# Kernel tuning notes

Measured on AMD Instinct MI355X. Metric: run time of the kernel, lower is better.

The kernel has to match this reference:

```python
import jax, jax.numpy as jnp
import numpy as np

B, T, T3, P = 512, 128, 64, 12
IN1, H1 = 64, 256
IN2, H2 = 64, 256
IN3, H3 = 32, 128
GLOB, OUT = 32, 2
FC_IN = 2 * H1 + H2 + GLOB + 2 * P * H3  # 3872


def lstm_last(x, Wih, Whh, bih, bhh):
    """Single-layer batch-first LSTM (PyTorch gate order i,f,g,o); returns last hidden state [B,H]."""
    Bx = x.shape[0]
    H = Whh.shape[1]
    # precompute input projections for all timesteps: [T, B, 4H]
    xg = jnp.swapaxes(jnp.einsum('bti,gi->btg', x, Wih) + bih + bhh, 0, 1)

    def step(carry, g):
        h, c = carry
        gates = g + h @ Whh.T
        i, f, gg, o = jnp.split(gates, 4, axis=-1)
        c = jax.nn.sigmoid(f) * c + jax.nn.sigmoid(i) * jnp.tanh(gg)
        h = jax.nn.sigmoid(o) * jnp.tanh(c)
        return (h, c), None

    h0 = jnp.zeros((Bx, H), x.dtype)
    (h, _), _ = jax.lax.scan(step, (h0, h0), xg)
    return h


def setup_inputs() -> dict:
    key = jax.random.key(0)
    ks = jax.random.split(key, 20)
    n = lambda k, s: jax.random.normal(k, s, dtype=jnp.float32)
    w = lambda k, s: jax.random.normal(k, s, dtype=jnp.float32) * 0.05
    return {
        'current_game': n(ks[0], (B, GLOB)),
        'games_home': n(ks[1], (B, T, IN1)),
        'games_away': n(ks[2], (B, T, IN1)),
        'games_vs': n(ks[3], (B, T, IN2)),
        'players_home': n(ks[4], (B, P, T3, IN3)),
        'players_away': n(ks[5], (B, P, T3, IN3)),
        'Wih1': w(ks[6], (4 * H1, IN1)), 'Whh1': w(ks[7], (4 * H1, H1)),
        'bih1': w(ks[8], (4 * H1,)), 'bhh1': w(ks[9], (4 * H1,)),
        'Wih2': w(ks[10], (4 * H2, IN2)), 'Whh2': w(ks[11], (4 * H2, H2)),
        'bih2': w(ks[12], (4 * H2,)), 'bhh2': w(ks[13], (4 * H2,)),
        'Wih3': w(ks[14], (4 * H3, IN3)), 'Whh3': w(ks[15], (4 * H3, H3)),
        'bih3': w(ks[16], (4 * H3,)), 'bhh3': w(ks[17], (4 * H3,)),
        'Wfc': w(ks[18], (OUT, FC_IN)), 'bfc': w(ks[19], (OUT,)),
    }


def reference(current_game, games_home, games_away, games_vs, players_home, players_away,
              Wih1, Whh1, bih1, bhh1, Wih2, Whh2, bih2, bhh2, Wih3, Whh3, bih3, bhh3,
              Wfc, bfc):
    h_home = lstm_last(games_home, Wih1, Whh1, bih1, bhh1)   # [B, H1]
    h_away = lstm_last(games_away, Wih1, Whh1, bih1, bhh1)   # shared rnn weights
    h_vs = lstm_last(games_vs, Wih2, Whh2, bih2, bhh2)       # [B, H2]

    def players_feat(xp):
        # fold the player dim into batch: one batched LSTM pass instead of P launches
        b, p = xp.shape[0], xp.shape[1]
        h = lstm_last(xp.reshape(b * p, xp.shape[2], xp.shape[3]), Wih3, Whh3, bih3, bhh3)
        return h.reshape(b, p * H3)  # concat in player order, matching the torch loop

    feat = jnp.concatenate([
        h_home, h_away, h_vs,
        players_feat(players_home), players_feat(players_away),
        current_game,
    ], axis=1)  # [B, FC_IN]
    return feat @ Wfc.T + bfc
```

## Files before the change

### kernel.cpp

```cpp
#include <hip/hip_runtime.h>
#include <stdint.h>

typedef __bf16 bf16;
typedef bf16 bf16x8 __attribute__((ext_vector_type(8)));
typedef bf16 bf16x4 __attribute__((ext_vector_type(4)));
typedef float f32x4 __attribute__((ext_vector_type(4)));
typedef int i32x4 __attribute__((ext_vector_type(4)));

#define DEV __device__ __forceinline__

static const size_t OFF_W1 = 0;
static const size_t OFF_W2 = OFF_W1 + (size_t)640 * 1024;
static const size_t OFF_W3 = OFF_W2 + (size_t)640 * 1024;
static const size_t OFF_B1 = OFF_W3 + (size_t)160 * 1024;
static const size_t OFF_B2 = OFF_B1 + 4096;
static const size_t OFF_B3 = OFF_B2 + 4096;
static const size_t OFF_FEAT = OFF_B3 + 2048;
static const size_t WS_NEEDED = OFF_FEAT + (size_t)512 * 3840 * 4;

DEV float sigm(float x) { return 1.f / (1.f + __expf(-x)); }
DEV float tanh_(float x) { return 1.f - 2.f / (__expf(2.f * x) + 1.f); }

DEV void mfma_bv(f32x4& acc, i32x4 a, i32x4 b) {
  asm("v_mfma_f32_16x16x32_bf16 %0, %1, %2, %0" : "+a"(acc) : "v"(a), "v"(b));
}
DEV void mfma_ba(f32x4& acc, i32x4 a, i32x4 b) {
  asm("v_mfma_f32_16x16x32_bf16 %0, %1, %2, %0" : "+a"(acc) : "v"(a), "a"(b));
}

template <int H, int IN, int NT, int NKT>
DEV void packW(const float* __restrict__ Wih, const float* __restrict__ Whh,
               bf16* __restrict__ dst, int i) {
  int e = i & 7, lane = (i >> 3) & 63;
  int rest = i >> 9;
  int kt = rest % NKT; rest /= NKT;
  int nt = rest % NT;  int w = rest / NT;
  int quad = lane >> 4, l16 = lane & 15;
  constexpr int NTG = NT / 4, UW = NT * 4;
  int unit = w * UW + (nt % NTG) * 16 + l16;
  int g = nt / NTG;
  int r = g * H + unit;
  int k = kt * 32 + quad * 8 + e;
  float v = (k < IN) ? Wih[r * IN + k] : Whh[r * H + (k - IN)];
  dst[i] = (bf16)v;
}

__global__ void prep_kernel(const float* __restrict__ Wih1, const float* __restrict__ Whh1,
                            const float* __restrict__ bih1, const float* __restrict__ bhh1,
                            const float* __restrict__ Wih2, const float* __restrict__ Whh2,
                            const float* __restrict__ bih2, const float* __restrict__ bhh2,
                            const float* __restrict__ Wih3, const float* __restrict__ Whh3,
                            const float* __restrict__ bih3, const float* __restrict__ bhh3,
                            uint8_t* __restrict__ ws) {
  const int gt = blockIdx.x * blockDim.x + threadIdx.x;
  const int gs = gridDim.x * blockDim.x;
  bf16* W1 = (bf16*)(ws + OFF_W1);
  bf16* W2 = (bf16*)(ws + OFF_W2);
  bf16* W3 = (bf16*)(ws + OFF_W3);
  float* B1 = (float*)(ws + OFF_B1);
  float* B2 = (float*)(ws + OFF_B2);
  float* B3 = (float*)(ws + OFF_B3);
  for (int i = gt; i < 640 * 512; i += gs) {
    packW<256, 64, 16, 10>(Wih1, Whh1, W1, i);
    packW<256, 64, 16, 10>(Wih2, Whh2, W2, i);
  }
  for (int i = gt; i < 160 * 512; i += gs) packW<128, 32, 8, 5>(Wih3, Whh3, W3, i);
  for (int i = gt; i < 1024; i += gs) { B1[i] = bih1[i] + bhh1[i]; B2[i] = bih2[i] + bhh2[i]; }
  for (int i = gt; i < 512; i += gs) B3[i] = bih3[i] + bhh3[i];
}

template <int BM, int IN, int H, int T, int NT, int NKT, int NVV, int NVA, int NL, int NS,
          int DOM>
DEV void lstm_tile3(const float* __restrict__ x0, const float* __restrict__ x1, int halfM,
                    const bf16* __restrict__ Wd, const float* __restrict__ bsum,
                    float* __restrict__ feat, int mg, uint8_t* smem) {
  static_assert(NVV + NVA + NL + NS == NT, "split");
  static_assert((NL == 0 && NS == 0) || (NKT % 2 == 0), "wrap parity");
  constexpr int MT = BM / 16;
  constexpr int NTG = NT / 4;
  constexpr int UW = NT * 4;
  constexpr int KCH = (IN + H) / 8;
  constexpr int SROW = KCH + 1;
  constexpr int AROWE = SROW * 8;
  constexpr int XPT = BM * IN / 4 / 256;

  const int tid = threadIdx.x;
  const int lane = tid & 63;
  const int w = tid >> 6;
  const int quad = lane >> 4;
  const int l16 = lane & 15;
  const int rowbase = mg * BM;

  bf16* A = (bf16*)smem;
  bf16* Wshm = (bf16*)(smem + (size_t)BM * AROWE * 2);

  const float* xb = (rowbase < halfM) ? x0 : x1;
  const int rowoff = rowbase - ((rowbase < halfM) ? 0 : halfM);

  {
    constexpr int HCH = KCH - IN / 8;
    for (int i = tid; i < BM * HCH * 4; i += 256) {
      int row = i / (HCH * 4), rem = i % (HCH * 4);
      int chunk = IN / 8 + rem / 4, d = rem % 4;
      ((uint32_t*)A)[row * SROW * 4 + chunk * 4 + d] = 0;
    }
  }
  if constexpr (NL > 0) {
    for (int idx = tid; idx < 4 * NL * NKT * 64; idx += 256) {
      int ln = idx & 63;
      int kt = (idx >> 6) % NKT;
      int rest = (idx >> 6) / NKT;
      int nl = rest % NL, w2 = rest / NL;
      int blob = (w2 * NT + NVV + NVA + nl) * NKT + kt;
      *(bf16x8*)(Wshm + (size_t)((w2 * NL + nl) * NKT + kt) * 512 + ln * 8) =
          *(const bf16x8*)(Wd + (size_t)blob * 512 + ln * 8);
    }
  }
  i32x4 wregv[NVV > 0 ? NVV : 1][NKT];
  {
    const bf16* Wv = Wd + (size_t)(w * NT) * NKT * 512 + lane * 8;
#pragma unroll
    for (int nt = 0; nt < NVV; ++nt)
#pragma unroll
      for (int kt = 0; kt < NKT; ++kt)
        wregv[nt][kt] = *(const i32x4*)(Wv + (size_t)(nt * NKT + kt) * 512);
  }
  i32x4 wrega[NVA > 0 ? NVA : 1][NKT];
  {
    const bf16* Wa = Wd + (size_t)(w * NT + NVV) * NKT * 512 + lane * 8;
#pragma unroll
    for (int nt = 0; nt < NVA; ++nt)
#pragma unroll
      for (int kt = 0; kt < NKT; ++kt)
        wrega[nt][kt] = *(const i32x4*)(Wa + (size_t)(nt * NKT + kt) * 512);
  }
  const bf16* Wstream = Wd + (size_t)(w * NT + NVV + NVA + NL) * NKT * 512 + lane * 8;

  float bias[4][NTG];
#pragma unroll
  for (int g = 0; g < 4; ++g)
#pragma unroll
    for (int ut = 0; ut < NTG; ++ut)
      bias[g][ut] = bsum[g * H + w * UW + ut * 16 + l16];

  i32x4 sbuf[2][NS > 0 ? NS : 1];
  i32x4 wlds[2][NL > 0 ? NL : 1];

  float4 xr[XPT];
#pragma unroll
  for (int i = 0; i < XPT; ++i) {
    int idx = i * 256 + tid;
    int row = idx / (IN / 4), c4 = idx % (IN / 4);
    xr[i] = *(const float4*)(xb + (size_t)(rowoff + row) * T * IN + c4 * 4);
  }
#pragma unroll
  for (int i = 0; i < XPT; ++i) {
    int idx = i * 256 + tid;
    int row = idx / (IN / 4), c4 = idx % (IN / 4);
    int k = c4 * 4;
    bf16x4 p;
    p[0] = (bf16)xr[i].x; p[1] = (bf16)xr[i].y; p[2] = (bf16)xr[i].z; p[3] = (bf16)xr[i].w;
    *(bf16x4*)(A + row * AROWE + (k >> 3) * 8 + (k & 7)) = p;
  }
  __syncthreads();
  if constexpr (NS > 0) {
#pragma unroll
    for (int ns = 0; ns < NS; ++ns)
      sbuf[0][ns] = *(const i32x4*)(Wstream + (size_t)(ns * NKT) * 512);
  }
  if constexpr (NL > 0) {
#pragma unroll
    for (int nl = 0; nl < NL; ++nl)
      wlds[0][nl] = *(const i32x4*)(Wshm + (size_t)((w * NL + nl) * NKT) * 512 + lane * 8);
  }

  float c[MT * NTG * 4];
#pragma unroll
  for (int i = 0; i < MT * NTG * 4; ++i) c[i] = 0.f;

  f32x4 acc[NT][MT];
#pragma unroll
  for (int nt = 0; nt < NT; ++nt)
#pragma unroll
    for (int mt = 0; mt < MT; ++mt) acc[nt][mt] = f32x4{0.f, 0.f, 0.f, 0.f};

  i32x4 afbuf[2][MT];

#pragma unroll 1
  for (int t = 0; t < T; ++t) {
#pragma unroll
    for (int mt = 0; mt < MT; ++mt)
      afbuf[0][mt] = *(const i32x4*)(A + (mt * 16 + l16) * AROWE + quad * 8);
    if (t < T - 1) {
#pragma unroll
      for (int i = 0; i < XPT; ++i) {
        int idx = i * 256 + tid;
        int row = idx / (IN / 4), c4 = idx % (IN / 4);
        xr[i] =
            *(const float4*)(xb + (size_t)(rowoff + row) * T * IN + (size_t)(t + 1) * IN + c4 * 4);
      }
    }
#pragma unroll
    for (int kt = 0; kt < NKT; ++kt) {
      const int ktn = (kt + 1) % NKT;
      const int pc = kt & 1, pn = (kt + 1) & 1;
      if (kt + 1 < NKT) {
#pragma unroll
        for (int mt = 0; mt < MT; ++mt)
          afbuf[pn][mt] = *(const i32x4*)(A + (mt * 16 + l16) * AROWE + ((kt + 1) * 4 + quad) * 8);
      }
      if constexpr (NS > 0) {
#pragma unroll
        for (int ns = 0; ns < NS; ++ns)
          sbuf[pn][ns] = *(const i32x4*)(Wstream + (size_t)(ns * NKT + ktn) * 512);
      }
      if constexpr (NL > 0) {
#pragma unroll
        for (int nl = 0; nl < NL; ++nl)
          wlds[pn][nl] = *(const i32x4*)(Wshm + (size_t)((w * NL + nl) * NKT + ktn) * 512 + lane * 8);
      }
#pragma unroll
      for (int nt = 0; nt < NVV; ++nt)
#pragma unroll
        for (int mt = 0; mt < MT; ++mt) mfma_bv(acc[nt][mt], afbuf[pc][mt], wregv[nt][kt]);
#pragma unroll
      for (int nt = 0; nt < NVA; ++nt)
#pragma unroll
        for (int mt = 0; mt < MT; ++mt) mfma_ba(acc[NVV + nt][mt], afbuf[pc][mt], wrega[nt][kt]);
      if constexpr (NL > 0) {
#pragma unroll
        for (int nl = 0; nl < NL; ++nl)
#pragma unroll
          for (int mt = 0; mt < MT; ++mt)
            mfma_bv(acc[NVV + NVA + nl][mt], afbuf[pc][mt], wlds[pc][nl]);
      }
      if constexpr (NS > 0) {
#pragma unroll
        for (int ns = 0; ns < NS; ++ns)
#pragma unroll
          for (int mt = 0; mt < MT; ++mt)
            mfma_bv(acc[NVV + NVA + NL + ns][mt], afbuf[pc][mt], sbuf[pc][ns]);
      }
    }
    __syncthreads();
    asm volatile("s_nop 7\n\ts_nop 7\n\ts_nop 7" ::);

#pragma unroll
    for (int mt = 0; mt < MT; ++mt)
#pragma unroll
      for (int ut = 0; ut < NTG; ++ut)
#pragma unroll
        for (int j = 0; j < 4; ++j) {
          float gi = acc[0 * NTG + ut][mt][j] + bias[0][ut];
          float gf = acc[1 * NTG + ut][mt][j] + bias[1][ut];
          float gg = acc[2 * NTG + ut][mt][j] + bias[2][ut];
          float go = acc[3 * NTG + ut][mt][j] + bias[3][ut];
          int ci = (mt * NTG + ut) * 4 + j;
          float cc = sigm(gf) * c[ci] + sigm(gi) * tanh_(gg);
          c[ci] = cc;
          float hv = sigm(go) * tanh_(cc);
          int row = mt * 16 + quad * 4 + j;
          if (t < T - 1) {
            int k = IN + w * UW + ut * 16 + l16;
            A[row * AROWE + (k >> 3) * 8 + (k & 7)] = (bf16)hv;
          } else {
            int R = rowbase + row;
            int unit = w * UW + ut * 16 + l16;
            int b, col;
            if (DOM == 0) {
              if (R < 512) { b = R; col = unit; }
              else         { b = R - 512; col = 256 + unit; }
            } else if (DOM == 1) {
              b = R; col = 512 + unit;
            } else {
              int rr = R; int base = 768;
              if (rr >= 6144) { rr -= 6144; base = 2304; }
              b = rr / 12; int p = rr - b * 12;
              col = base + p * 128 + unit;
            }
            feat[(size_t)b * 3840 + col] = hv;
          }
        }
#pragma unroll
    for (int nt = 0; nt < NT; ++nt)
#pragma unroll
      for (int mt = 0; mt < MT; ++mt) acc[nt][mt] = f32x4{0.f, 0.f, 0.f, 0.f};
    if (t < T - 1) {
#pragma unroll
      for (int i = 0; i < XPT; ++i) {
        int idx = i * 256 + tid;
        int row = idx / (IN / 4), c4 = idx % (IN / 4);
        int k = c4 * 4;
        bf16x4 p;
        p[0] = (bf16)xr[i].x; p[1] = (bf16)xr[i].y; p[2] = (bf16)xr[i].z; p[3] = (bf16)xr[i].w;
        *(bf16x4*)(A + row * AROWE + (k >> 3) * 8 + (k & 7)) = p;
      }
    }
    __syncthreads();
  }
}

template <int NL1, int NS1>
DEV void lstm_body(const float* gh, const float* ga, const float* gv, const float* ph,
                   const float* pa, uint8_t* ws, uint8_t* smem) {
  float* feat = (float*)(ws + OFF_FEAT);
  int bid = blockIdx.x;
  if (bid < 64) {
    lstm_tile3<16, 64, 256, 128, 16, 10, 2, 4, NL1, NS1, 0>(
        gh, ga, 512, (const bf16*)(ws + OFF_W1), (const float*)(ws + OFF_B1), feat, bid, smem);
  } else if (bid < 96) {
    lstm_tile3<16, 64, 256, 128, 16, 10, 2, 4, NL1, NS1, 1>(
        gv, gv, 512, (const bf16*)(ws + OFF_W2), (const float*)(ws + OFF_B2), feat, bid - 64, smem);
  } else {
    lstm_tile3<64, 32, 128, 64, 8, 5, 3, 5, 0, 0, 2>(
        ph, pa, 6144, (const bf16*)(ws + OFF_W3), (const float*)(ws + OFF_B3), feat, bid - 96, smem);
  }
}

__global__ __launch_bounds__(256, 1) void lstm_main_big(const float* __restrict__ gh,
                                                        const float* __restrict__ ga,
                                                        const float* __restrict__ gv,
                                                        const float* __restrict__ ph,
                                                        const float* __restrict__ pa,
                                                        uint8_t* __restrict__ ws) {
  extern __shared__ uint8_t smem[];
  lstm_body<2, 8>(gh, ga, gv, ph, pa, ws, smem);
}

__global__ __launch_bounds__(256, 1) void lstm_main_small(const float* __restrict__ gh,
                                                          const float* __restrict__ ga,
                                                          const float* __restrict__ gv,
                                                          const float* __restrict__ ph,
                                                          const float* __restrict__ pa,
                                                          uint8_t* __restrict__ ws) {
  extern __shared__ uint8_t smem[];
  lstm_body<1, 9>(gh, ga, gv, ph, pa, ws, smem);
}

__global__ void fc_kernel(const float* __restrict__ feat, const float* __restrict__ cg,
                          const float* __restrict__ Wfc, const float* __restrict__ bfc,
                          float* __restrict__ out) {
  int b = blockIdx.x, tid = threadIdx.x;
  float a0 = 0.f, a1 = 0.f;
  for (int c = tid; c < 3840; c += 256) {
    float f = feat[(size_t)b * 3840 + c];
    a0 += f * Wfc[c];
    a1 += f * Wfc[3872 + c];
  }
  if (tid < 32) {
    float f = cg[b * 32 + tid];
    a0 += f * Wfc[3840 + tid];
    a1 += f * Wfc[3872 + 3840 + tid];
  }
#pragma unroll
  for (int o = 32; o > 0; o >>= 1) {
    a0 += __shfl_down(a0, o);
    a1 += __shfl_down(a1, o);
  }
  __shared__ float red[8];
  int wv = tid >> 6;
  if ((tid & 63) == 0) { red[wv * 2] = a0; red[wv * 2 + 1] = a1; }
  __syncthreads();
  if (tid == 0) {
    out[b * 2 + 0] = red[0] + red[2] + red[4] + red[6] + bfc[0];
    out[b * 2 + 1] = red[1] + red[3] + red[5] + red[7] + bfc[1];
  }
}

extern "C" void kernel_launch(void* const* d_in, const int* in_sizes, int n_in, void* d_out,
                              int out_size, void* d_ws, size_t ws_size, hipStream_t stream) {
  const float* cg = (const float*)d_in[0];
  const float* gh = (const float*)d_in[1];
  const float* ga = (const float*)d_in[2];
  const float* gv = (const float*)d_in[3];
  const float* ph = (const float*)d_in[4];
  const float* pa = (const float*)d_in[5];
  const float* Wih1 = (const float*)d_in[6];
  const float* Whh1 = (const float*)d_in[7];
  const float* bih1 = (const float*)d_in[8];
  const float* bhh1 = (const float*)d_in[9];
  const float* Wih2 = (const float*)d_in[10];
  const float* Whh2 = (const float*)d_in[11];
  const float* bih2 = (const float*)d_in[12];
  const float* bhh2 = (const float*)d_in[13];
  const float* Wih3 = (const float*)d_in[14];
  const float* Whh3 = (const float*)d_in[15];
  const float* bih3 = (const float*)d_in[16];
  const float* bhh3 = (const float*)d_in[17];
  const float* Wfc = (const float*)d_in[18];
  const float* bfc = (const float*)d_in[19];
  uint8_t* ws = (uint8_t*)d_ws;
  if (ws_size < WS_NEEDED) return;

  hipLaunchKernelGGL(prep_kernel, dim3(512), dim3(256), 0, stream, Wih1, Whh1, bih1, bhh1,
                     Wih2, Whh2, bih2, bhh2, Wih3, Whh3, bih3, bhh3, ws);

  int dev = 0, maxShm = 0;
  (void)hipGetDevice(&dev);
  (void)hipDeviceGetAttribute(&maxShm, hipDeviceAttributeMaxSharedMemoryPerBlock, dev);
  hipError_t ae = hipFuncSetAttribute((const void*)lstm_main_big,
                                      hipFuncAttributeMaxDynamicSharedMemorySize, 92416);
  if (ae == hipSuccess && maxShm >= 92416) {
    hipLaunchKernelGGL(lstm_main_big, dim3(288), dim3(256), 92416, stream, gh, ga, gv, ph, pa, ws);
  } else {
    hipLaunchKernelGGL(lstm_main_small, dim3(288), dim3(256), 51456, stream, gh, ga, gv, ph, pa,
                       ws);
  }
  hipLaunchKernelGGL(fc_kernel, dim3(512), dim3(256), 0, stream,
                     (const float*)(ws + OFF_FEAT), cg, Wfc, bfc, (float*)d_out);
}
```

Baseline: 1.928 ms.

## Double LSTM batch tile for big LSTMs, switch to fp16 MFMA, fold bias into accumulator init

The H=256 LSTMs now process 32 rows per block instead of 16, halving block count (288 to 240 blocks) and doubling weight reuse per streamed weight fragment. The weight split is rebalanced toward LDS (more weights in shared memory, fewer in registers) and shared memory grows to about 140KB. Operands switch from bf16 to fp16 for better mantissa precision, and bias is preloaded into the accumulators rather than added in the gate epilogue. The risk is more register pressure and longer per-step MFMA chains per block on the serial recurrence.

```diff
diff --git a/kernel.cpp b/kernel.cpp
--- a/kernel.cpp
+++ b/kernel.cpp
@@ -1,9 +1,9 @@
 #include <hip/hip_runtime.h>
 #include <stdint.h>
 
-typedef __bf16 bf16;
-typedef bf16 bf16x8 __attribute__((ext_vector_type(8)));
-typedef bf16 bf16x4 __attribute__((ext_vector_type(4)));
+typedef _Float16 f16;
+typedef f16 f16x8 __attribute__((ext_vector_type(8)));
+typedef f16 f16x4 __attribute__((ext_vector_type(4)));
 typedef float f32x4 __attribute__((ext_vector_type(4)));
 typedef int i32x4 __attribute__((ext_vector_type(4)));
 
@@ -22,15 +22,15 @@
 DEV float tanh_(float x) { return 1.f - 2.f / (__expf(2.f * x) + 1.f); }
 
 DEV void mfma_bv(f32x4& acc, i32x4 a, i32x4 b) {
-  asm("v_mfma_f32_16x16x32_bf16 %0, %1, %2, %0" : "+a"(acc) : "v"(a), "v"(b));
+  asm("v_mfma_f32_16x16x32_f16 %0, %1, %2, %0" : "+a"(acc) : "v"(a), "v"(b));
 }
 DEV void mfma_ba(f32x4& acc, i32x4 a, i32x4 b) {
-  asm("v_mfma_f32_16x16x32_bf16 %0, %1, %2, %0" : "+a"(acc) : "v"(a), "a"(b));
+  asm("v_mfma_f32_16x16x32_f16 %0, %1, %2, %0" : "+a"(acc) : "v"(a), "a"(b));
 }
 
 template <int H, int IN, int NT, int NKT>
 DEV void packW(const float* __restrict__ Wih, const float* __restrict__ Whh,
-               bf16* __restrict__ dst, int i) {
+               f16* __restrict__ dst, int i) {
   int e = i & 7, lane = (i >> 3) & 63;
   int rest = i >> 9;
   int kt = rest % NKT; rest /= NKT;
@@ -42,7 +42,7 @@
   int r = g * H + unit;
   int k = kt * 32 + quad * 8 + e;
   float v = (k < IN) ? Wih[r * IN + k] : Whh[r * H + (k - IN)];
-  dst[i] = (bf16)v;
+  dst[i] = (f16)v;
 }
 
 __global__ void prep_kernel(const float* __restrict__ Wih1, const float* __restrict__ Whh1,
@@ -54,9 +54,9 @@
                             uint8_t* __restrict__ ws) {
   const int gt = blockIdx.x * blockDim.x + threadIdx.x;
   const int gs = gridDim.x * blockDim.x;
-  bf16* W1 = (bf16*)(ws + OFF_W1);
-  bf16* W2 = (bf16*)(ws + OFF_W2);
-  bf16* W3 = (bf16*)(ws + OFF_W3);
+  f16* W1 = (f16*)(ws + OFF_W1);
+  f16* W2 = (f16*)(ws + OFF_W2);
+  f16* W3 = (f16*)(ws + OFF_W3);
   float* B1 = (float*)(ws + OFF_B1);
   float* B2 = (float*)(ws + OFF_B2);
   float* B3 = (float*)(ws + OFF_B3);
@@ -71,8 +71,8 @@
 
 template <int BM, int IN, int H, int T, int NT, int NKT, int NVV, int NVA, int NL, int NS,
           int DOM>
-DEV void lstm_tile3(const float* __restrict__ x0, const float* __restrict__ x1, int halfM,
-                    const bf16* __restrict__ Wd, const float* __restrict__ bsum,
+DEV void lstm_tile5(const float* __restrict__ x0, const float* __restrict__ x1, int halfM,
+                    const f16* __restrict__ Wd, const float* __restrict__ bsum,
                     float* __restrict__ feat, int mg, uint8_t* smem) {
   static_assert(NVV + NVA + NL + NS == NT, "split");
   static_assert((NL == 0 && NS == 0) || (NKT % 2 == 0), "wrap parity");
@@ -91,8 +91,8 @@
   const int l16 = lane & 15;
   const int rowbase = mg * BM;
 
-  bf16* A = (bf16*)smem;
-  bf16* Wshm = (bf16*)(smem + (size_t)BM * AROWE * 2);
+  f16* A = (f16*)smem;
+  f16* Wshm = (f16*)(smem + (size_t)BM * AROWE * 2);
 
   const float* xb = (rowbase < halfM) ? x0 : x1;
   const int rowoff = rowbase - ((rowbase < halfM) ? 0 : halfM);
@@ -112,13 +112,13 @@
       int rest = (idx >> 6) / NKT;
       int nl = rest % NL, w2 = rest / NL;
       int blob = (w2 * NT + NVV + NVA + nl) * NKT + kt;
-      *(bf16x8*)(Wshm + (size_t)((w2 * NL + nl) * NKT + kt) * 512 + ln * 8) =
-          *(const bf16x8*)(Wd + (size_t)blob * 512 + ln * 8);
+      *(i32x4*)(Wshm + (size_t)((w2 * NL + nl) * NKT + kt) * 512 + ln * 8) =
+          *(const i32x4*)(Wd + (size_t)blob * 512 + ln * 8);
     }
   }
   i32x4 wregv[NVV > 0 ? NVV : 1][NKT];
   {
-    const bf16* Wv = Wd + (size_t)(w * NT) * NKT * 512 + lane * 8;
+    const f16* Wv = Wd + (size_t)(w * NT) * NKT * 512 + lane * 8;
 #pragma unroll
     for (int nt = 0; nt < NVV; ++nt)
 #pragma unroll
@@ -127,21 +127,19 @@
   }
   i32x4 wrega[NVA > 0 ? NVA : 1][NKT];
   {
-    const bf16* Wa = Wd + (size_t)(w * NT + NVV) * NKT * 512 + lane * 8;
+    const f16* Wa = Wd + (size_t)(w * NT + NVV) * NKT * 512 + lane * 8;
 #pragma unroll
     for (int nt = 0; nt < NVA; ++nt)
 #pragma unroll
       for (int kt = 0; kt < NKT; ++kt)
         wrega[nt][kt] = *(const i32x4*)(Wa + (size_t)(nt * NKT + kt) * 512);
   }
-  const bf16* Wstream = Wd + (size_t)(w * NT + NVV + NVA + NL) * NKT * 512 + lane * 8;
-
-  float bias[4][NTG];
-#pragma unroll
-  for (int g = 0; g < 4; ++g)
-#pragma unroll
-    for (int ut = 0; ut < NTG; ++ut)
-      bias[g][ut] = bsum[g * H + w * UW + ut * 16 + l16];
+  const f16* Wstream = Wd + (size_t)(w * NT + NVV + NVA + NL) * NKT * 512 + lane * 8;
+
+  float bias[NT];
+#pragma unroll
+  for (int nt = 0; nt < NT; ++nt)
+    bias[nt] = bsum[(nt / NTG) * H + w * UW + (nt % NTG) * 16 + l16];
 
   i32x4 sbuf[2][NS > 0 ? NS : 1];
   i32x4 wlds[2][NL > 0 ? NL : 1];
@@ -158,9 +156,9 @@
     int idx = i * 256 + tid;
     int row = idx / (IN / 4), c4 = idx % (IN / 4);
     int k = c4 * 4;
-    bf16x4 p;
-    p[0] = (bf16)xr[i].x; p[1] = (bf16)xr[i].y; p[2] = (bf16)xr[i].z; p[3] = (bf16)xr[i].w;
-    *(bf16x4*)(A + row * AROWE + (k >> 3) * 8 + (k & 7)) = p;
+    f16x4 p;
+    p[0] = (f16)xr[i].x; p[1] = (f16)xr[i].y; p[2] = (f16)xr[i].z; p[3] = (f16)xr[i].w;
+    *(f16x4*)(A + row * AROWE + (k >> 3) * 8 + (k & 7)) = p;
   }
   __syncthreads();
   if constexpr (NS > 0) {
@@ -182,7 +180,8 @@
 #pragma unroll
   for (int nt = 0; nt < NT; ++nt)
 #pragma unroll
-    for (int mt = 0; mt < MT; ++mt) acc[nt][mt] = f32x4{0.f, 0.f, 0.f, 0.f};
+    for (int mt = 0; mt < MT; ++mt)
+      acc[nt][mt] = f32x4{bias[nt], bias[nt], bias[nt], bias[nt]};
 
   i32x4 afbuf[2][MT];
 
@@ -202,8 +201,8 @@
     }
 #pragma unroll
     for (int kt = 0; kt < NKT; ++kt) {
+      const int pc = kt & 1, pn = (kt + 1) & 1;
       const int ktn = (kt + 1) % NKT;
-      const int pc = kt & 1, pn = (kt + 1) & 1;
       if (kt + 1 < NKT) {
 #pragma unroll
         for (int mt = 0; mt < MT; ++mt)
@@ -251,10 +250,10 @@
       for (int ut = 0; ut < NTG; ++ut)
 #pragma unroll
         for (int j = 0; j < 4; ++j) {
-          float gi = acc[0 * NTG + ut][mt][j] + bias[0][ut];
-          float gf = acc[1 * NTG + ut][mt][j] + bias[1][ut];
-          float gg = acc[2 * NTG + ut][mt][j] + bias[2][ut];
-          float go = acc[3 * NTG + ut][mt][j] + bias[3][ut];
+          float gi = acc[0 * NTG + ut][mt][j];
+          float gf = acc[1 * NTG + ut][mt][j];
+          float gg = acc[2 * NTG + ut][mt][j];
+          float go = acc[3 * NTG + ut][mt][j];
           int ci = (mt * NTG + ut) * 4 + j;
           float cc = sigm(gf) * c[ci] + sigm(gi) * tanh_(gg);
           c[ci] = cc;
@@ -262,7 +261,7 @@
           int row = mt * 16 + quad * 4 + j;
           if (t < T - 1) {
             int k = IN + w * UW + ut * 16 + l16;
-            A[row * AROWE + (k >> 3) * 8 + (k & 7)] = (bf16)hv;
+            A[row * AROWE + (k >> 3) * 8 + (k & 7)] = (f16)hv;
           } else {
             int R = rowbase + row;
             int unit = w * UW + ut * 16 + l16;
@@ -284,16 +283,17 @@
 #pragma unroll
     for (int nt = 0; nt < NT; ++nt)
 #pragma unroll
-      for (int mt = 0; mt < MT; ++mt) acc[nt][mt] = f32x4{0.f, 0.f, 0.f, 0.f};
+      for (int mt = 0; mt < MT; ++mt)
+        acc[nt][mt] = f32x4{bias[nt], bias[nt], bias[nt], bias[nt]};
     if (t < T - 1) {
 #pragma unroll
       for (int i = 0; i < XPT; ++i) {
         int idx = i * 256 + tid;
         int row = idx / (IN / 4), c4 = idx % (IN / 4);
         int k = c4 * 4;
-        bf16x4 p;
-        p[0] = (bf16)xr[i].x; p[1] = (bf16)xr[i].y; p[2] = (bf16)xr[i].z; p[3] = (bf16)xr[i].w;
-        *(bf16x4*)(A + row * AROWE + (k >> 3) * 8 + (k & 7)) = p;
+        f16x4 p;
+        p[0] = (f16)xr[i].x; p[1] = (f16)xr[i].y; p[2] = (f16)xr[i].z; p[3] = (f16)xr[i].w;
+        *(f16x4*)(A + row * AROWE + (k >> 3) * 8 + (k & 7)) = p;
       }
     }
     __syncthreads();
@@ -305,15 +305,15 @@
                    const float* pa, uint8_t* ws, uint8_t* smem) {
   float* feat = (float*)(ws + OFF_FEAT);
   int bid = blockIdx.x;
-  if (bid < 64) {
-    lstm_tile3<16, 64, 256, 128, 16, 10, 2, 4, NL1, NS1, 0>(
-        gh, ga, 512, (const bf16*)(ws + OFF_W1), (const float*)(ws + OFF_B1), feat, bid, smem);
-  } else if (bid < 96) {
-    lstm_tile3<16, 64, 256, 128, 16, 10, 2, 4, NL1, NS1, 1>(
-        gv, gv, 512, (const bf16*)(ws + OFF_W2), (const float*)(ws + OFF_B2), feat, bid - 64, smem);
+  if (bid < 32) {
+    lstm_tile5<32, 64, 256, 128, 16, 10, 1, 3, NL1, NS1, 0>(
+        gh, ga, 512, (const f16*)(ws + OFF_W1), (const float*)(ws + OFF_B1), feat, bid, smem);
+  } else if (bid < 48) {
+    lstm_tile5<32, 64, 256, 128, 16, 10, 1, 3, NL1, NS1, 1>(
+        gv, gv, 512, (const f16*)(ws + OFF_W2), (const float*)(ws + OFF_B2), feat, bid - 32, smem);
   } else {
-    lstm_tile3<64, 32, 128, 64, 8, 5, 3, 5, 0, 0, 2>(
-        ph, pa, 6144, (const bf16*)(ws + OFF_W3), (const float*)(ws + OFF_B3), feat, bid - 96, smem);
+    lstm_tile5<64, 32, 128, 64, 8, 5, 3, 5, 0, 0, 2>(
+        ph, pa, 6144, (const f16*)(ws + OFF_W3), (const float*)(ws + OFF_B3), feat, bid - 48, smem);
   }
 }
 
@@ -324,7 +324,7 @@
                                                         const float* __restrict__ pa,
                                                         uint8_t* __restrict__ ws) {
   extern __shared__ uint8_t smem[];
-  lstm_body<2, 8>(gh, ga, gv, ph, pa, ws, smem);
+  lstm_body<3, 9>(gh, ga, gv, ph, pa, ws, smem);
 }
 
 __global__ __launch_bounds__(256, 1) void lstm_main_small(const float* __restrict__ gh,
@@ -334,7 +334,7 @@
                                                           const float* __restrict__ pa,
                                                           uint8_t* __restrict__ ws) {
   extern __shared__ uint8_t smem[];
-  lstm_body<1, 9>(gh, ga, gv, ph, pa, ws, smem);
+  lstm_body<1, 11>(gh, ga, gv, ph, pa, ws, smem);
 }
 
 __global__ void fc_kernel(const float* __restrict__ feat, const float* __restrict__ cg,
@@ -399,11 +399,11 @@
   (void)hipGetDevice(&dev);
   (void)hipDeviceGetAttribute(&maxShm, hipDeviceAttributeMaxSharedMemoryPerBlock, dev);
   hipError_t ae = hipFuncSetAttribute((const void*)lstm_main_big,
-                                      hipFuncAttributeMaxDynamicSharedMemorySize, 92416);
-  if (ae == hipSuccess && maxShm >= 92416) {
-    hipLaunchKernelGGL(lstm_main_big, dim3(288), dim3(256), 92416, stream, gh, ga, gv, ph, pa, ws);
+                                      hipFuncAttributeMaxDynamicSharedMemorySize, 143872);
+  if (ae == hipSuccess && maxShm >= 143872) {
+    hipLaunchKernelGGL(lstm_main_big, dim3(240), dim3(256), 143872, stream, gh, ga, gv, ph, pa, ws);
   } else {
-    hipLaunchKernelGGL(lstm_main_small, dim3(288), dim3(256), 51456, stream, gh, ga, gv, ph, pa,
+    hipLaunchKernelGGL(lstm_main_small, dim3(240), dim3(256), 61952, stream, gh, ga, gv, ph, pa,
                        ws);
   }
   hipLaunchKernelGGL(fc_kernel, dim3(512), dim3(256), 0, stream,
```

Result: slower. 3.330 ms (+72.7%).
